# Kernel optimization log

Measured on AMD Instinct MI355X. Metric: run time of the kernel, lower is better.

## Reference

```python
import jax, jax.numpy as jnp
import numpy as np

N_TOKENS = 262144
TOP_K = 2
N_EXPERTS = 8
D_IN = 128
D_OUT = 128


def setup_inputs() -> dict:
    key = jax.random.key(0)
    k1, k2, k3, k4 = jax.random.split(key, 4)
    inputs = jax.random.normal(k1, (N_TOKENS, D_IN), dtype=jnp.float32)
    # nn.Parameter weight: [num_experts, output_size, input_size]
    weight = jax.random.normal(k2, (N_EXPERTS, D_OUT, D_IN), dtype=jnp.float32) * 0.02
    gates = jax.random.uniform(k3, (N_TOKENS, TOP_K), dtype=jnp.float32)
    # raw expert assignment per (token, slot); sorted/argsorted as the kernel expects
    raw_experts = jax.random.randint(k4, (N_TOKENS * TOP_K,), 0, N_EXPERTS, dtype=jnp.int32)
    sorted_expert_idxs = jnp.sort(raw_experts)
    sorted_scattered_idxs = jnp.argsort(raw_experts, stable=True).astype(jnp.int32)
    padded_block_idxs = jnp.arange(N_TOKENS * TOP_K, dtype=jnp.int32)  # kernel-internal, unused in math
    return {
        "inputs": inputs,
        "weight": weight,
        "gates": gates,
        "k": TOP_K,
        "sorted_expert_idxs": sorted_expert_idxs,
        "sorted_scattered_idxs": sorted_scattered_idxs,
        "padded_block_idxs": padded_block_idxs,
    }


def _scatter2scatter(inputs, w_eio, k, sorted_expert_idxs, sorted_scattered_idxs):
    """x_grouped=False, y_grouped=False path of scattermoe scatter2scatter.
    inputs: [N, d_in]; w_eio: [E, d_in, d_out]; returns [N*k, d_out] in original slot order.
    """
    # gather input rows in expert-sorted order
    x_sorted = inputs[sorted_scattered_idxs // k]  # [N*k, d_in]
    n_experts = w_eio.shape[0]
    y_sorted = jnp.zeros((x_sorted.shape[0], w_eio.shape[2]), dtype=x_sorted.dtype)
    for e in range(n_experts):  # small fixed expert count
        mask = (sorted_expert_idxs == e)[:, None]
        y_sorted = y_sorted + jnp.where(mask, x_sorted, 0.0) @ w_eio[e]
    # scatter back to original flat [N*k] slot order
    return jnp.zeros_like(y_sorted).at[sorted_scattered_idxs].set(y_sorted)


def reference(inputs, weight, gates, k, sorted_expert_idxs, sorted_scattered_idxs, padded_block_idxs):
    w_eio = jnp.transpose(weight, (0, 2, 1))  # [E, d_in, d_out], matches weight.permute(0, 2, 1)
    output = _scatter2scatter(inputs, w_eio, k, sorted_expert_idxs, sorted_scattered_idxs)
    # gated combine: bmm(gates.unsqueeze(1), output.view(N, k, d_out)).squeeze(1)
    n, kk = gates.shape
    expanded = output.reshape(n, kk, -1)
    return jnp.einsum("nk,nkd->nd", gates, expanded)
```

## Files before the change

kernel.cpp:

```cpp
#include <hip/hip_runtime.h>


#define D       128
#define TILE_P  128
#define LSTR    136
#define NTOK    262144
#define NK      (NTOK * 2)

typedef _Float16 halfx8 __attribute__((ext_vector_type(8)));
typedef _Float16 halfx4 __attribute__((ext_vector_type(4)));
typedef _Float16 halfx2 __attribute__((ext_vector_type(2)));
typedef float    floatx4 __attribute__((ext_vector_type(4)));

__device__ __forceinline__ void load_bfrag(const float* __restrict__ weight,
                                           int e, int c0, int m, int q,
                                           halfx8 bf[2][4])
{
    #pragma unroll
    for (int ct = 0; ct < 2; ++ct) {
        const int o = c0 + 2 * m + ct;
        const float* wrow = weight + (size_t)e * (D * D) + (size_t)o * D;
        #pragma unroll
        for (int ks = 0; ks < 4; ++ks) {
            const int col = ks * 32 + q * 8;
            float4 v0 = *(const float4*)(wrow + col);
            float4 v1 = *(const float4*)(wrow + col + 4);
            halfx8 h = { (_Float16)v0.x, (_Float16)v0.y, (_Float16)v0.z, (_Float16)v0.w,
                         (_Float16)v1.x, (_Float16)v1.y, (_Float16)v1.z, (_Float16)v1.w };
            bf[ct][ks] = h;
        }
    }
}

__global__ __launch_bounds__(256, 4)
void moe_mfma_kernel(const float* __restrict__ inputs,
                     const float* __restrict__ weight,
                     const float* __restrict__ gates,
                     const int*   __restrict__ sei,
                     const int*   __restrict__ ssi,
                     _Float16*    __restrict__ ws)
{
    __shared__ _Float16 As[TILE_P * LSTR];
    __shared__ int   toks[TILE_P];
    __shared__ int   slots[TILE_P];
    __shared__ float gts[TILE_P];
    __shared__ int   eids[TILE_P];

    const int tid = threadIdx.x;
    const int p0  = blockIdx.x * TILE_P;

    if (tid < TILE_P) {
        int s = ssi[p0 + tid];
        slots[tid] = s;
        toks[tid]  = s >> 1;
        gts[tid]   = gates[s];
        eids[tid]  = sei[p0 + tid];
    }
    __syncthreads();

    #pragma unroll
    for (int it = 0; it < 16; ++it) {
        int id = it * 256 + tid;
        int r  = id >> 5;
        int c4 = id & 31;
        float4 v = ((const float4*)inputs)[(size_t)toks[r] * 32 + c4];
        halfx4 h = { (_Float16)v.x, (_Float16)v.y, (_Float16)v.z, (_Float16)v.w };
        *(halfx4*)&As[r * LSTR + c4 * 4] = h;
    }

    const int uniform = __syncthreads_and((tid >= TILE_P) || (eids[tid] == eids[0]));

    const int lane = tid & 63;
    const int w    = tid >> 6;
    const int m    = lane & 15;
    const int q    = lane >> 4;
    const int c0   = w * 32;

    floatx4 acc[8][2];
    #pragma unroll
    for (int rt = 0; rt < 8; ++rt) {
        acc[rt][0] = {0.f, 0.f, 0.f, 0.f};
        acc[rt][1] = {0.f, 0.f, 0.f, 0.f};
    }

    if (uniform) {
        halfx8 bf[2][4];
        load_bfrag(weight, eids[0], c0, m, q, bf);
        #pragma unroll
        for (int ks = 0; ks < 4; ++ks) {
            const int kk = ks * 32 + q * 8;
            #pragma unroll
            for (int rt = 0; rt < 8; ++rt) {
                halfx8 a = *(const halfx8*)&As[(rt * 16 + m) * LSTR + kk];
                acc[rt][0] = __builtin_amdgcn_mfma_f32_16x16x32_f16(a, bf[0][ks], acc[rt][0], 0, 0, 0);
                acc[rt][1] = __builtin_amdgcn_mfma_f32_16x16x32_f16(a, bf[1][ks], acc[rt][1], 0, 0, 0);
            }
        }
    } else {
        int s0 = 0;
        while (s0 < TILE_P) {
            int e = eids[s0], s1 = s0 + 1;
            while (s1 < TILE_P && eids[s1] == e) ++s1;
            halfx8 bf[2][4];
            load_bfrag(weight, e, c0, m, q, bf);
            #pragma unroll
            for (int ks = 0; ks < 4; ++ks) {
                const int kk = ks * 32 + q * 8;
                #pragma unroll
                for (int rt = 0; rt < 8; ++rt) {
                    const int row = rt * 16 + m;
                    halfx8 a = {0,0,0,0,0,0,0,0};
                    if (row >= s0 && row < s1)
                        a = *(const halfx8*)&As[row * LSTR + kk];
                    acc[rt][0] = __builtin_amdgcn_mfma_f32_16x16x32_f16(a, bf[0][ks], acc[rt][0], 0, 0, 0);
                    acc[rt][1] = __builtin_amdgcn_mfma_f32_16x16x32_f16(a, bf[1][ks], acc[rt][1], 0, 0, 0);
                }
            }
            s0 = s1;
        }
    }

    __syncthreads();
    _Float16* Y = As;

    #pragma unroll
    for (int rt = 0; rt < 8; ++rt) {
        #pragma unroll
        for (int r = 0; r < 4; ++r) {
            int row = rt * 16 + q * 4 + r;
            float g = gts[row];
            halfx2 h = { (_Float16)(acc[rt][0][r] * g),
                         (_Float16)(acc[rt][1][r] * g) };
            *(halfx2*)&Y[row * LSTR + c0 + 2 * m] = h;
        }
    }
    __syncthreads();

    #pragma unroll
    for (int it = 0; it < 8; ++it) {
        int seg = it * 256 + tid;
        int row = seg >> 4;
        int c8  = (seg & 15) * 8;
        halfx8 v = *(const halfx8*)&Y[row * LSTR + c8];
        *(halfx8*)(ws + (size_t)slots[row] * D + c8) = v;
    }
}

__global__ __launch_bounds__(256)
void combine_kernel(const _Float16* __restrict__ ws, float* __restrict__ out)
{
    int gid = blockIdx.x * 256 + threadIdx.x;
    int t = gid >> 4;
    int j = (gid & 15) * 8;
    halfx8 a = *(const halfx8*)(ws + (size_t)(2 * t) * D + j);
    halfx8 b = *(const halfx8*)(ws + (size_t)(2 * t + 1) * D + j);
    float* dst = out + (size_t)t * D + j;
    float4 lo = { (float)a[0] + (float)b[0], (float)a[1] + (float)b[1],
                  (float)a[2] + (float)b[2], (float)a[3] + (float)b[3] };
    float4 hi = { (float)a[4] + (float)b[4], (float)a[5] + (float)b[5],
                  (float)a[6] + (float)b[6], (float)a[7] + (float)b[7] };
    *(float4*)dst = lo;
    *(float4*)(dst + 4) = hi;
}

extern "C" void kernel_launch(void* const* d_in, const int* in_sizes, int n_in,
                              void* d_out, int out_size, void* d_ws, size_t ws_size,
                              hipStream_t stream)
{
    const float* inputs = (const float*)d_in[0];
    const float* weight = (const float*)d_in[1];
    const float* gates  = (const float*)d_in[2];
    const int*   sei    = (const int*)d_in[4];
    const int*   ssi    = (const int*)d_in[5];
    float*    out = (float*)d_out;
    _Float16* ws  = (_Float16*)d_ws;

    moe_mfma_kernel<<<dim3(NK / TILE_P), dim3(256), 0, stream>>>(
        inputs, weight, gates, sei, ssi, ws);

    combine_kernel<<<dim3(NTOK * 16 / 256), dim3(256), 0, stream>>>(ws, out);
}
```

Measured before the change: 341.1 us.

## Fuse expert GEMM and gated combine per token tile via inverse expert map

Adds a prep kernel that builds a per-slot expert byte map from the sorted indices and converts the weights to fp16 once. The main kernel now processes 64 contiguous tokens (128 slots) per block. It buckets slots by expert in shared memory with atomics and runs MFMA per expert segment. It then sums the two gated slot outputs directly into the fp32 output. This removes the fp16 intermediate workspace round trip, the separate combine kernel, and the random gather of input rows. In exchange, every block now handles up to 8 expert segments with partial tiles, which wastes MFMA work, and it adds an extra prep launch with a scattered byte write.

```diff
diff --git a/kernel.cpp b/kernel.cpp
--- a/kernel.cpp
+++ b/kernel.cpp
@@ -2,79 +2,98 @@
 
 
 #define D       128
-#define TILE_P  128
+#define TB      64
+#define SLOTS   128
 #define LSTR    136
 #define NTOK    262144
 #define NK      (NTOK * 2)
+#define NEXP    8
 
 typedef _Float16 halfx8 __attribute__((ext_vector_type(8)));
 typedef _Float16 halfx4 __attribute__((ext_vector_type(4)));
 typedef _Float16 halfx2 __attribute__((ext_vector_type(2)));
 typedef float    floatx4 __attribute__((ext_vector_type(4)));
 
-__device__ __forceinline__ void load_bfrag(const float* __restrict__ weight,
-                                           int e, int c0, int m, int q,
-                                           halfx8 bf[2][4])
+__global__ __launch_bounds__(256)
+void prep_kernel(const int* __restrict__ sei, const int* __restrict__ ssi,
+                 const float* __restrict__ weight,
+                 unsigned char* __restrict__ inv, _Float16* __restrict__ wh)
 {
-    #pragma unroll
-    for (int ct = 0; ct < 2; ++ct) {
-        const int o = c0 + 2 * m + ct;
-        const float* wrow = weight + (size_t)e * (D * D) + (size_t)o * D;
-        #pragma unroll
-        for (int ks = 0; ks < 4; ++ks) {
-            const int col = ks * 32 + q * 8;
-            float4 v0 = *(const float4*)(wrow + col);
-            float4 v1 = *(const float4*)(wrow + col + 4);
-            halfx8 h = { (_Float16)v0.x, (_Float16)v0.y, (_Float16)v0.z, (_Float16)v0.w,
-                         (_Float16)v1.x, (_Float16)v1.y, (_Float16)v1.z, (_Float16)v1.w };
-            bf[ct][ks] = h;
-        }
+    const int b = blockIdx.x, tid = threadIdx.x;
+    if (b < NK / 256) {
+        const int p = b * 256 + tid;
+        inv[ssi[p]] = (unsigned char)sei[p];
+    } else {
+        const int i = ((b - NK / 256) * 256 + tid) * 4;
+        float4 v = *(const float4*)(weight + i);
+        halfx4 h = { (_Float16)v.x, (_Float16)v.y, (_Float16)v.z, (_Float16)v.w };
+        *(halfx4*)(wh + i) = h;
     }
 }
 
 __global__ __launch_bounds__(256, 4)
-void moe_mfma_kernel(const float* __restrict__ inputs,
-                     const float* __restrict__ weight,
-                     const float* __restrict__ gates,
-                     const int*   __restrict__ sei,
-                     const int*   __restrict__ ssi,
-                     _Float16*    __restrict__ ws)
+void moe_fused_kernel(const float* __restrict__ inputs,
+                      const _Float16* __restrict__ wh,
+                      const float* __restrict__ gates,
+                      const unsigned char* __restrict__ inv,
+                      float* __restrict__ out)
 {
-    __shared__ _Float16 As[TILE_P * LSTR];
-    __shared__ int   toks[TILE_P];
-    __shared__ int   slots[TILE_P];
-    __shared__ float gts[TILE_P];
-    __shared__ int   eids[TILE_P];
+    __shared__ _Float16 As[SLOTS * LSTR];
+    __shared__ int   atok[SLOTS];
+    __shared__ int   posOf[SLOTS];
+    __shared__ float gs[SLOTS];
+    __shared__ int   cnt[NEXP];
+    __shared__ int   ebase[NEXP + 1];
 
     const int tid = threadIdx.x;
-    const int p0  = blockIdx.x * TILE_P;
+    const int t0  = blockIdx.x * TB;
 
-    if (tid < TILE_P) {
-        int s = ssi[p0 + tid];
-        slots[tid] = s;
-        toks[tid]  = s >> 1;
-        gts[tid]   = gates[s];
-        eids[tid]  = sei[p0 + tid];
+    if (tid < NEXP) cnt[tid] = 0;
+    __syncthreads();
+
+    int myE = 0, myR = 0; float myG = 0.f;
+    if (tid < SLOTS) {
+        myE = inv[(size_t)t0 * 2 + tid];
+        myG = gates[(size_t)t0 * 2 + tid];
+        myR = atomicAdd(&cnt[myE], 1);
+    }
+
+    #pragma unroll
+    for (int it = 0; it < 8; ++it) {
+        const int id = it * 256 + tid;
+        const int r  = id >> 5;
+        const int c4 = id & 31;
+        float4 v = ((const float4*)inputs)[(size_t)(t0 + r) * 32 + c4];
+        halfx4 h = { (_Float16)v.x, (_Float16)v.y, (_Float16)v.z, (_Float16)v.w };
+        *(halfx4*)&As[r * LSTR + c4 * 4] = h;
     }
     __syncthreads();
 
-    #pragma unroll
-    for (int it = 0; it < 16; ++it) {
-        int id = it * 256 + tid;
-        int r  = id >> 5;
-        int c4 = id & 31;
-        float4 v = ((const float4*)inputs)[(size_t)toks[r] * 32 + c4];
-        halfx4 h = { (_Float16)v.x, (_Float16)v.y, (_Float16)v.z, (_Float16)v.w };
-        *(halfx4*)&As[r * LSTR + c4 * 4] = h;
+    if (tid == 0) {
+        int a = 0;
+        #pragma unroll
+        for (int e = 0; e < NEXP; ++e) { ebase[e] = a; a += cnt[e]; }
+        ebase[NEXP] = a;
     }
+    __syncthreads();
 
-    const int uniform = __syncthreads_and((tid >= TILE_P) || (eids[tid] == eids[0]));
+    if (tid < SLOTS) {
+        const int p = ebase[myE] + myR;
+        posOf[tid] = p;
+        atok[p]    = tid >> 1;
+        gs[p]      = myG;
+    }
+    __syncthreads();
 
     const int lane = tid & 63;
     const int w    = tid >> 6;
     const int m    = lane & 15;
     const int q    = lane >> 4;
     const int c0   = w * 32;
+
+    int aoff[8];
+    #pragma unroll
+    for (int rt = 0; rt < 8; ++rt) aoff[rt] = atok[rt * 16 + m] * LSTR;
 
     floatx4 acc[8][2];
     #pragma unroll
@@ -83,40 +102,34 @@
         acc[rt][1] = {0.f, 0.f, 0.f, 0.f};
     }
 
-    if (uniform) {
+    for (int e = 0; e < NEXP; ++e) {
+        const int s0 = ebase[e], s1 = ebase[e + 1];
+        if (s0 == s1) continue;
+
         halfx8 bf[2][4];
-        load_bfrag(weight, eids[0], c0, m, q, bf);
         #pragma unroll
-        for (int ks = 0; ks < 4; ++ks) {
-            const int kk = ks * 32 + q * 8;
+        for (int ct = 0; ct < 2; ++ct) {
+            const _Float16* wrow = wh + (size_t)e * (D * D)
+                                      + (size_t)(c0 + 2 * m + ct) * D;
             #pragma unroll
-            for (int rt = 0; rt < 8; ++rt) {
-                halfx8 a = *(const halfx8*)&As[(rt * 16 + m) * LSTR + kk];
+            for (int ks = 0; ks < 4; ++ks)
+                bf[ct][ks] = *(const halfx8*)(wrow + ks * 32 + q * 8);
+        }
+
+        const int rt_lo = s0 >> 4, rt_hi = (s1 - 1) >> 4;
+        #pragma unroll
+        for (int rt = 0; rt < 8; ++rt) {
+            if (rt < rt_lo || rt > rt_hi) continue;
+            const int row = rt * 16 + m;
+            const bool in = (row >= s0) && (row < s1);
+            #pragma unroll
+            for (int ks = 0; ks < 4; ++ks) {
+                const int kk = ks * 32 + q * 8;
+                halfx8 a = {0, 0, 0, 0, 0, 0, 0, 0};
+                if (in) a = *(const halfx8*)&As[aoff[rt] + kk];
                 acc[rt][0] = __builtin_amdgcn_mfma_f32_16x16x32_f16(a, bf[0][ks], acc[rt][0], 0, 0, 0);
                 acc[rt][1] = __builtin_amdgcn_mfma_f32_16x16x32_f16(a, bf[1][ks], acc[rt][1], 0, 0, 0);
             }
-        }
-    } else {
-        int s0 = 0;
-        while (s0 < TILE_P) {
-            int e = eids[s0], s1 = s0 + 1;
-            while (s1 < TILE_P && eids[s1] == e) ++s1;
-            halfx8 bf[2][4];
-            load_bfrag(weight, e, c0, m, q, bf);
-            #pragma unroll
-            for (int ks = 0; ks < 4; ++ks) {
-                const int kk = ks * 32 + q * 8;
-                #pragma unroll
-                for (int rt = 0; rt < 8; ++rt) {
-                    const int row = rt * 16 + m;
-                    halfx8 a = {0,0,0,0,0,0,0,0};
-                    if (row >= s0 && row < s1)
-                        a = *(const halfx8*)&As[row * LSTR + kk];
-                    acc[rt][0] = __builtin_amdgcn_mfma_f32_16x16x32_f16(a, bf[0][ks], acc[rt][0], 0, 0, 0);
-                    acc[rt][1] = __builtin_amdgcn_mfma_f32_16x16x32_f16(a, bf[1][ks], acc[rt][1], 0, 0, 0);
-                }
-            }
-            s0 = s1;
         }
     }
 
@@ -127,8 +140,8 @@
     for (int rt = 0; rt < 8; ++rt) {
         #pragma unroll
         for (int r = 0; r < 4; ++r) {
-            int row = rt * 16 + q * 4 + r;
-            float g = gts[row];
+            const int row = rt * 16 + q * 4 + r;
+            const float g = gs[row];
             halfx2 h = { (_Float16)(acc[rt][0][r] * g),
                          (_Float16)(acc[rt][1][r] * g) };
             *(halfx2*)&Y[row * LSTR + c0 + 2 * m] = h;
@@ -137,30 +150,22 @@
     __syncthreads();
 
     #pragma unroll
-    for (int it = 0; it < 8; ++it) {
-        int seg = it * 256 + tid;
-        int row = seg >> 4;
-        int c8  = (seg & 15) * 8;
-        halfx8 v = *(const halfx8*)&Y[row * LSTR + c8];
-        *(halfx8*)(ws + (size_t)slots[row] * D + c8) = v;
+    for (int it = 0; it < 4; ++it) {
+        const int idx = it * 256 + tid;
+        const int r   = idx >> 4;
+        const int c8  = (idx & 15) * 8;
+        const int p0  = posOf[2 * r];
+        const int p1  = posOf[2 * r + 1];
+        halfx8 a = *(const halfx8*)&Y[p0 * LSTR + c8];
+        halfx8 b = *(const halfx8*)&Y[p1 * LSTR + c8];
+        float* dst = out + (size_t)(t0 + r) * D + c8;
+        float4 lo = { (float)a[0] + (float)b[0], (float)a[1] + (float)b[1],
+                      (float)a[2] + (float)b[2], (float)a[3] + (float)b[3] };
+        float4 hi = { (float)a[4] + (float)b[4], (float)a[5] + (float)b[5],
+                      (float)a[6] + (float)b[6], (float)a[7] + (float)b[7] };
+        *(float4*)dst = lo;
+        *(float4*)(dst + 4) = hi;
     }
-}
-
-__global__ __launch_bounds__(256)
-void combine_kernel(const _Float16* __restrict__ ws, float* __restrict__ out)
-{
-    int gid = blockIdx.x * 256 + threadIdx.x;
-    int t = gid >> 4;
-    int j = (gid & 15) * 8;
-    halfx8 a = *(const halfx8*)(ws + (size_t)(2 * t) * D + j);
-    halfx8 b = *(const halfx8*)(ws + (size_t)(2 * t + 1) * D + j);
-    float* dst = out + (size_t)t * D + j;
-    float4 lo = { (float)a[0] + (float)b[0], (float)a[1] + (float)b[1],
-                  (float)a[2] + (float)b[2], (float)a[3] + (float)b[3] };
-    float4 hi = { (float)a[4] + (float)b[4], (float)a[5] + (float)b[5],
-                  (float)a[6] + (float)b[6], (float)a[7] + (float)b[7] };
-    *(float4*)dst = lo;
-    *(float4*)(dst + 4) = hi;
 }
 
 extern "C" void kernel_launch(void* const* d_in, const int* in_sizes, int n_in,
@@ -172,11 +177,14 @@
     const float* gates  = (const float*)d_in[2];
     const int*   sei    = (const int*)d_in[4];
     const int*   ssi    = (const int*)d_in[5];
-    float*    out = (float*)d_out;
-    _Float16* ws  = (_Float16*)d_ws;
+    float* out = (float*)d_out;
 
-    moe_mfma_kernel<<<dim3(NK / TILE_P), dim3(256), 0, stream>>>(
-        inputs, weight, gates, sei, ssi, ws);
+    unsigned char* inv = (unsigned char*)d_ws;
+    _Float16*      wh  = (_Float16*)((char*)d_ws + NK);
 
-    combine_kernel<<<dim3(NTOK * 16 / 256), dim3(256), 0, stream>>>(ws, out);
+    prep_kernel<<<dim3(NK / 256 + (NEXP * D * D) / 1024), dim3(256), 0, stream>>>(
+        sei, ssi, weight, inv, wh);
+
+    moe_fused_kernel<<<dim3(NTOK / TB), dim3(256), 0, stream>>>(
+        inputs, wh, gates, inv, out);
 }
```

Result: faster. 333.6 us (-2.2%).
